# Kernel optimization log

Measured on AMD Instinct MI355X. Metric: run time of the kernel, lower is better.

The kernel has to match this reference:

```python
import jax, jax.numpy as jnp
import numpy as np

PI = 3.141592653589793
N, B, DIM, HEADS = 4, 8192, 1024, 4
HD = DIM // HEADS  # head_dim = 256


def setup_inputs() -> dict:
    key = jax.random.key(0)
    ks = jax.random.split(key, 10)
    glorot = jax.nn.initializers.glorot_uniform()
    return {
        "axis_embeddings": jax.random.normal(ks[0], (N, B, DIM), jnp.float32),
        "arg_embeddings": jax.random.uniform(ks[1], (N, B, DIM), jnp.float32),
        "W_axis1": glorot(ks[2], (HD, 2 * HD), jnp.float32),
        "b_axis1": jnp.zeros((HD,), jnp.float32),
        "W_arg1": glorot(ks[3], (HD, 2 * HD), jnp.float32),
        "b_arg1": jnp.zeros((HD,), jnp.float32),
        "W_axis2": glorot(ks[4], (HD, HD), jnp.float32),
        "b_axis2": jnp.zeros((HD,), jnp.float32),
        "W_arg2": glorot(ks[5], (HD, HD), jnp.float32),
        "b_arg2": jnp.zeros((HD,), jnp.float32),
    }


def _linear(x, W, b):
    return jnp.einsum('...i,oi->...o', x, W) + b


def reference(axis_embeddings, arg_embeddings, W_axis1, b_axis1, W_arg1, b_arg1,
              W_axis2, b_axis2, W_arg2, b_arg2):
    axis = axis_embeddings.reshape(N, B, HEADS, HD)
    arg = arg_embeddings.reshape(N, B, HEADS, HD)
    al = axis - arg / 2
    ah = axis + arg / 2
    logits = jnp.concatenate([al, ah], axis=-1)  # [N,B,H,2*HD]

    # axis branch: attention over N then circular mean via atan2-style correction
    axis_h1 = jax.nn.relu(_linear(logits, W_axis1, b_axis1))
    axis_attn = jax.nn.softmax(_linear(axis_h1, W_axis2, b_axis2), axis=0)
    x_emb = jnp.sum(axis_attn * jnp.cos(axis), axis=0)  # [B,H,HD]
    y_emb = jnp.sum(axis_attn * jnp.sin(axis), axis=0)
    x_emb = jnp.where(jnp.abs(x_emb) < 0.001, 0.001, x_emb)
    axis_out = jnp.arctan(y_emb / x_emb)
    ind_x = x_emb < 0
    ind_y = y_emb < 0
    ind_two = ind_x & jnp.logical_not(ind_y)
    ind_three = ind_x & ind_y
    axis_out = axis_out + PI * ind_two.astype(axis_out.dtype) - PI * ind_three.astype(axis_out.dtype)

    # arg branch: mean-pooled gate, min over N (dropout p=0 -> identity)
    arg_h1 = jax.nn.relu(_linear(logits, W_arg1, b_arg1))
    gate = jax.nn.sigmoid(_linear(jnp.mean(arg_h1, axis=0), W_arg2, b_arg2))
    arg_out = jnp.min(arg, axis=0) * gate

    return axis_out.reshape(B, DIM), arg_out.reshape(B, DIM)
```

## Files before the change

kernel.cpp:

```cpp
#include <hip/hip_runtime.h>


typedef __attribute__((ext_vector_type(8))) _Float16 f16x8;
typedef __attribute__((ext_vector_type(8))) float f32x8;
typedef __attribute__((ext_vector_type(4))) float f32x4;

#define BH 32768
#define OUT_ARG_OFF 8388608

#define O_WXA_H 0
#define O_WXA_L 65536
#define O_WXR_H 131072
#define O_WXR_L 196608
#define O_WRA_H 262144
#define O_WRR_H 327680
#define O_W2X_H 393216
#define O_W2X_L 458752
#define O_W2G_H 524288
#define WS_HALFS 589824

__device__ __forceinline__ void split16(float x, _Float16& hi, _Float16& lo) {
  float xs = x * 16.0f;
  _Float16 h = (_Float16)xs;
  hi = h;
  lo = (_Float16)(xs - (float)h);
}

__device__ __forceinline__ int fragidx(int o, int k) {
  int ct = o >> 4, kk = k >> 5, lg = (k >> 3) & 3, l15 = o & 15, j = k & 7;
  return (ct * 8 + kk) * 512 + (lg * 16 + l15) * 8 + j;
}

__global__ void combine_weights(const float* __restrict__ Wx1, const float* __restrict__ Wr1,
                                const float* __restrict__ W2x, const float* __restrict__ W2g,
                                _Float16* __restrict__ ws) {
  int i = blockIdx.x * 256 + threadIdx.x;
  int o = i >> 8, k = i & 255;
  int d = fragidx(o, k);
  float a = Wx1[o * 512 + k], b = Wx1[o * 512 + 256 + k];
  _Float16 h, l;
  split16(a + b, h, l);          ws[O_WXA_H + d] = h; ws[O_WXA_L + d] = l;
  split16(0.5f * (b - a), h, l); ws[O_WXR_H + d] = h; ws[O_WXR_L + d] = l;
  a = Wr1[o * 512 + k]; b = Wr1[o * 512 + 256 + k];
  ws[O_WRA_H + d] = (_Float16)((a + b) * 16.0f);
  ws[O_WRR_H + d] = (_Float16)((0.5f * (b - a)) * 16.0f);
  split16(W2x[o * 256 + k], h, l); ws[O_W2X_H + d] = h; ws[O_W2X_L + d] = l;
  ws[O_W2G_H + d] = (_Float16)(W2g[o * 256 + k] * 16.0f);
}

#define MFMA16 __builtin_amdgcn_mfma_f32_16x16x32_f16

__global__ __launch_bounds__(512, 2)
void cone_main(const float* __restrict__ axisF, const float* __restrict__ argF,
               const float* __restrict__ bx1, const float* __restrict__ br1,
               const float* __restrict__ bg2,
               const _Float16* __restrict__ ws, float* __restrict__ out)
{
  __shared__ __align__(16) _Float16 lds[32768];
  _Float16* bufAxH = lds;
  _Float16* bufAxL = lds + 8192;
  _Float16* bufArH = lds + 16384;
  _Float16* bufArL = lds + 24576;

  const int tid = threadIdx.x;
  const int w   = tid >> 6;
  const int l   = tid & 63;
  const int l15 = l & 15;
  const int lg  = l >> 4;
  int bid = blockIdx.x;
  bid = ((bid & 7) << 9) + (bid >> 3);
  const int g0 = bid << 3;
  const float s = 1.0f / 256.0f;

  {
    #pragma unroll
    for (int c = 0; c < 2; ++c) {
      const int i   = c * 512 + tid;
      const int row = i >> 5;
      const int col = (i & 31) * 8;
      const int gofs = ((row & 3) * BH + g0 + (row >> 2)) * 256 + col;
      f32x8 va = *(const f32x8*)(axisF + gofs);
      f32x8 vr = *(const f32x8*)(argF + gofs);
      f16x8 xh, xl, rh, rl;
      #pragma unroll
      for (int j = 0; j < 8; ++j) {
        _Float16 h, lo2;
        split16(va[j], h, lo2); xh[j] = h; xl[j] = lo2;
        split16(vr[j], h, lo2); rh[j] = h; rl[j] = lo2;
      }
      const int ad = row * 256 + (col ^ ((row & 7) << 3));
      *(f16x8*)(bufAxH + ad) = xh;
      *(f16x8*)(bufAxL + ad) = xl;
      *(f16x8*)(bufArH + ad) = rh;
      *(f16x8*)(bufArL + ad) = rl;
    }
  }
  __syncthreads();

  f32x4 acc1[2][2], accm[2][2];
  #pragma unroll
  for (int mt = 0; mt < 2; ++mt)
    #pragma unroll
    for (int nt = 0; nt < 2; ++nt) { acc1[mt][nt] = (f32x4){0,0,0,0}; accm[mt][nt] = (f32x4){0,0,0,0}; }

  const int ct0 = w << 1;

  #pragma unroll
  for (int kk = 0; kk < 8; ++kk) {
    f16x8 xh[2], xl[2], rh[2], rl[2];
    #pragma unroll
    for (int mt = 0; mt < 2; ++mt) {
      const int row = (mt << 4) + l15;
      const int ad  = row * 256 + ((((kk) << 5) + (lg << 3)) ^ ((row & 7) << 3));
      xh[mt] = *(const f16x8*)(bufAxH + ad);
      xl[mt] = *(const f16x8*)(bufAxL + ad);
      rh[mt] = *(const f16x8*)(bufArH + ad);
      rl[mt] = *(const f16x8*)(bufArL + ad);
    }
    #pragma unroll
    for (int nt = 0; nt < 2; ++nt) {
      const int fb = (((ct0 + nt) << 3) + kk) * 512 + l * 8;
      const f16x8 wxah = *(const f16x8*)(ws + O_WXA_H + fb);
      const f16x8 wxal = *(const f16x8*)(ws + O_WXA_L + fb);
      const f16x8 wraw = *(const f16x8*)(ws + O_WRA_H + fb);
      const f16x8 wxrh = *(const f16x8*)(ws + O_WXR_H + fb);
      const f16x8 wxrl = *(const f16x8*)(ws + O_WXR_L + fb);
      const f16x8 wrrw = *(const f16x8*)(ws + O_WRR_H + fb);
      __builtin_amdgcn_s_setprio(1);
      #pragma unroll
      for (int mt = 0; mt < 2; ++mt) {
        acc1[mt][nt] = MFMA16(xh[mt], wxah, acc1[mt][nt], 0, 0, 0);
        acc1[mt][nt] = MFMA16(xl[mt], wxah, acc1[mt][nt], 0, 0, 0);
        acc1[mt][nt] = MFMA16(xh[mt], wxal, acc1[mt][nt], 0, 0, 0);
        accm[mt][nt] = MFMA16(xh[mt], wraw, accm[mt][nt], 0, 0, 0);
        acc1[mt][nt] = MFMA16(rh[mt], wxrh, acc1[mt][nt], 0, 0, 0);
        acc1[mt][nt] = MFMA16(rl[mt], wxrh, acc1[mt][nt], 0, 0, 0);
        acc1[mt][nt] = MFMA16(rh[mt], wxrl, acc1[mt][nt], 0, 0, 0);
        accm[mt][nt] = MFMA16(rh[mt], wrrw, accm[mt][nt], 0, 0, 0);
      }
      __builtin_amdgcn_s_setprio(0);
    }
  }
  __syncthreads();

  _Float16* h1h = bufAxH;
  _Float16* h1l = bufAxL;
  _Float16* h1m = bufArH;
  if (tid < 256) *(f16x8*)(h1m + 2048 + tid * 8) = (f16x8){0,0,0,0,0,0,0,0};
  #pragma unroll
  for (int nt = 0; nt < 2; ++nt) {
    const int c  = (w << 5) + (nt << 4) + l15;
    const float bvx = bx1[c];
    const float bvr = br1[c];
    #pragma unroll
    for (int mt = 0; mt < 2; ++mt) {
      #pragma unroll
      for (int r = 0; r < 4; ++r) {
        const int row = (mt << 4) + (lg << 2) + r;
        const float v = fmaxf(acc1[mt][nt][r] * s + bvx, 0.f);
        _Float16 h, lo2; split16(v, h, lo2);
        const int ad = row * 256 + (c ^ ((row & 7) << 3));
        h1h[ad] = h; h1l[ad] = lo2;
      }
      const int p = (mt << 2) + lg;
      float sm = 0.f;
      #pragma unroll
      for (int r = 0; r < 4; ++r) sm += fmaxf(accm[mt][nt][r] * s + bvr, 0.f);
      h1m[p * 256 + (c ^ ((p & 7) << 3))] = (_Float16)(0.25f * sm * 16.0f);
    }
  }
  __syncthreads();

  f32x4 acc2[2][2];
  f32x4 acc3[2];
  #pragma unroll
  for (int mt = 0; mt < 2; ++mt) { acc2[mt][0] = (f32x4){0,0,0,0}; acc2[mt][1] = (f32x4){0,0,0,0}; }
  acc3[0] = (f32x4){0,0,0,0}; acc3[1] = (f32x4){0,0,0,0};
  {
    f16x8 wh[3][2], wl[3][2], wg[3][2];
    f16x8 a2h[2][2], a2l[2][2], am[2];
    #pragma unroll
    for (int p = 0; p < 2; ++p)
      #pragma unroll
      for (int nt = 0; nt < 2; ++nt) {
        const int fb = (((ct0 + nt) << 3) + p) * 512 + l * 8;
        wh[p][nt] = *(const f16x8*)(ws + O_W2X_H + fb);
        wl[p][nt] = *(const f16x8*)(ws + O_W2X_L + fb);
        wg[p][nt] = *(const f16x8*)(ws + O_W2G_H + fb);
      }
    #pragma unroll
    for (int mt = 0; mt < 2; ++mt) {
      const int row = (mt << 4) + l15;
      const int ad  = row * 256 + ((lg << 3) ^ ((row & 7) << 3));
      a2h[0][mt] = *(const f16x8*)(h1h + ad);
      a2l[0][mt] = *(const f16x8*)(h1l + ad);
    }
    am[0] = *(const f16x8*)(h1m + l15 * 256 + ((lg << 3) ^ ((l15 & 7) << 3)));
    #pragma unroll
    for (int kk = 0; kk < 8; ++kk) {
      const int cs = kk % 3, ns = (kk + 2) % 3, ab = kk & 1, an = ab ^ 1;
      if (kk < 6) {
        #pragma unroll
        for (int nt = 0; nt < 2; ++nt) {
          const int fb = (((ct0 + nt) << 3) + (kk + 2)) * 512 + l * 8;
          wh[ns][nt] = *(const f16x8*)(ws + O_W2X_H + fb);
          wl[ns][nt] = *(const f16x8*)(ws + O_W2X_L + fb);
          wg[ns][nt] = *(const f16x8*)(ws + O_W2G_H + fb);
        }
      }
      if (kk < 7) {
        #pragma unroll
        for (int mt = 0; mt < 2; ++mt) {
          const int row = (mt << 4) + l15;
          const int ad  = row * 256 + ((((kk + 1) << 5) + (lg << 3)) ^ ((row & 7) << 3));
          a2h[an][mt] = *(const f16x8*)(h1h + ad);
          a2l[an][mt] = *(const f16x8*)(h1l + ad);
        }
        am[an] = *(const f16x8*)(h1m + l15 * 256 + ((((kk + 1) << 5) + (lg << 3)) ^ ((l15 & 7) << 3)));
      }
      __builtin_amdgcn_s_setprio(1);
      #pragma unroll
      for (int nt = 0; nt < 2; ++nt) {
        #pragma unroll
        for (int mt = 0; mt < 2; ++mt) {
          acc2[mt][nt] = MFMA16(a2h[ab][mt], wh[cs][nt], acc2[mt][nt], 0, 0, 0);
          acc2[mt][nt] = MFMA16(a2l[ab][mt], wh[cs][nt], acc2[mt][nt], 0, 0, 0);
          acc2[mt][nt] = MFMA16(a2h[ab][mt], wl[cs][nt], acc2[mt][nt], 0, 0, 0);
        }
        acc3[nt] = MFMA16(am[ab], wg[cs][nt], acc3[nt], 0, 0, 0);
      }
      __builtin_amdgcn_s_setprio(0);
    }
  }

  #pragma unroll
  for (int nt = 0; nt < 2; ++nt) {
    const int c = (w << 5) + (nt << 4) + l15;
    #pragma unroll
    for (int mt = 0; mt < 2; ++mt) {
      float lv[4];
      #pragma unroll
      for (int r = 0; r < 4; ++r) lv[r] = acc2[mt][nt][r] * s;
      const float mx = fmaxf(fmaxf(lv[0], lv[1]), fmaxf(lv[2], lv[3]));
      float e[4]; float sum = 0.f;
      #pragma unroll
      for (int r = 0; r < 4; ++r) { e[r] = __expf(lv[r] - mx); sum += e[r]; }
      const float inv = 1.f / sum;
      const int g = g0 + (mt << 2) + lg;
      float x = 0.f, y = 0.f;
      #pragma unroll
      for (int r = 0; r < 4; ++r) {
        const float av = axisF[(r * BH + g) * 256 + c];
        float sn, cs2;
        __sincosf(av, &sn, &cs2);
        const float at = e[r] * inv;
        x += at * cs2;
        y += at * sn;
      }
      if (fabsf(x) < 0.001f) x = 0.001f;
      out[g * 256 + c] = atan2f(y, x);
    }
  }

  #pragma unroll
  for (int nt = 0; nt < 2; ++nt) {
    const int c = (w << 5) + (nt << 4) + l15;
    const float bgv = bg2[c];
    #pragma unroll
    for (int r = 0; r < 4; ++r) {
      const int p = (lg << 2) + r;
      if (p < 8) {
        const int g = g0 + p;
        const float gate = 1.f / (1.f + __expf(-(acc3[nt][r] * s + bgv)));
        float mn = argF[g * 256 + c];
        #pragma unroll
        for (int n = 1; n < 4; ++n)
          mn = fminf(mn, argF[(n * BH + g) * 256 + c]);
        out[OUT_ARG_OFF + g * 256 + c] = mn * gate;
      }
    }
  }
}

extern "C" void kernel_launch(void* const* d_in, const int* in_sizes, int n_in,
                              void* d_out, int out_size, void* d_ws, size_t ws_size,
                              hipStream_t stream) {
  const float* axisF = (const float*)d_in[0];
  const float* argF  = (const float*)d_in[1];
  const float* Wx1   = (const float*)d_in[2];
  const float* bx1   = (const float*)d_in[3];
  const float* Wr1   = (const float*)d_in[4];
  const float* br1   = (const float*)d_in[5];
  const float* W2x   = (const float*)d_in[6];
  const float* W2g   = (const float*)d_in[8];
  const float* bg2   = (const float*)d_in[9];
  float* out = (float*)d_out;
  _Float16* ws = (_Float16*)d_ws;

  combine_weights<<<256, 256, 0, stream>>>(Wx1, Wr1, W2x, W2g, ws);
  cone_main<<<4096, 512, 0, stream>>>(axisF, argF, bx1, br1, bg2, ws, out);
}
```

Before: 324.5 us.

## Switch main GEMMs to 32x32x16 MFMA tiles with new fragment layout

Reworks the first-layer and axis second-layer GEMMs to use 32x32x16 f16 MFMA instructions with a single 32x32 accumulator per wave, repacking weights into a 32-wide fragment layout and widening the LDS XOR swizzle to 32 rows. Weight fragments are double-buffered from global memory across the k loop, and epilogue global loads for axis and arg values are batched before use. The aim is fewer MFMA issues and fewer LDS fragment reads per unit of work, with better latency hiding. The bigger accumulators raise register pressure, and the new swizzle and layout must stay consistent between the staging writes and the fragment reads.

```diff
diff --git a/kernel.cpp b/kernel.cpp
--- a/kernel.cpp
+++ b/kernel.cpp
@@ -4,6 +4,7 @@
 typedef __attribute__((ext_vector_type(8))) _Float16 f16x8;
 typedef __attribute__((ext_vector_type(8))) float f32x8;
 typedef __attribute__((ext_vector_type(4))) float f32x4;
+typedef __attribute__((ext_vector_type(16))) float f32x16;
 
 #define BH 32768
 #define OUT_ARG_OFF 8388608
@@ -26,9 +27,11 @@
   lo = (_Float16)(xs - (float)h);
 }
 
-__device__ __forceinline__ int fragidx(int o, int k) {
-  int ct = o >> 4, kk = k >> 5, lg = (k >> 3) & 3, l15 = o & 15, j = k & 7;
-  return (ct * 8 + kk) * 512 + (lg * 16 + l15) * 8 + j;
+__device__ __forceinline__ int fragidx16(int o, int k) {
+  return ((o >> 4) * 8 + (k >> 5)) * 512 + ((((k >> 3) & 3) << 4) + (o & 15)) * 8 + (k & 7);
+}
+__device__ __forceinline__ int fragidx32(int o, int k) {
+  return ((o >> 5) * 16 + (k >> 4)) * 512 + ((((k >> 3) & 1) << 5) + (o & 31)) * 8 + (k & 7);
 }
 
 __global__ void combine_weights(const float* __restrict__ Wx1, const float* __restrict__ Wr1,
@@ -36,7 +39,7 @@
                                 _Float16* __restrict__ ws) {
   int i = blockIdx.x * 256 + threadIdx.x;
   int o = i >> 8, k = i & 255;
-  int d = fragidx(o, k);
+  int d = fragidx32(o, k);
   float a = Wx1[o * 512 + k], b = Wx1[o * 512 + 256 + k];
   _Float16 h, l;
   split16(a + b, h, l);          ws[O_WXA_H + d] = h; ws[O_WXA_L + d] = l;
@@ -45,10 +48,44 @@
   ws[O_WRA_H + d] = (_Float16)((a + b) * 16.0f);
   ws[O_WRR_H + d] = (_Float16)((0.5f * (b - a)) * 16.0f);
   split16(W2x[o * 256 + k], h, l); ws[O_W2X_H + d] = h; ws[O_W2X_L + d] = l;
-  ws[O_W2G_H + d] = (_Float16)(W2g[o * 256 + k] * 16.0f);
+  ws[O_W2G_H + fragidx16(o, k)] = (_Float16)(W2g[o * 256 + k] * 16.0f);
 }
 
 #define MFMA16 __builtin_amdgcn_mfma_f32_16x16x32_f16
+#define MFMA32 __builtin_amdgcn_mfma_f32_32x32x16_f16
+
+__device__ __forceinline__ void gemm1_pass32(const _Float16* __restrict__ ws,
+                                             int oBh, int oBl, int oBm,
+                                             const _Float16* bufH, const _Float16* bufL,
+                                             int w, int l,
+                                             f32x16& acc1, f32x16& accm) {
+  const int row = l & 31;
+  const int hi8 = (l >> 5) << 3;
+  f16x8 wh[2], wl[2], wm[2];
+  {
+    const int fb = (w * 16) * 512 + l * 8;
+    wh[0] = *(const f16x8*)(ws + oBh + fb);
+    wl[0] = *(const f16x8*)(ws + oBl + fb);
+    wm[0] = *(const f16x8*)(ws + oBm + fb);
+  }
+  #pragma unroll
+  for (int st = 0; st < 16; ++st) {
+    const int cur = st & 1, nx = cur ^ 1;
+    if (st < 15) {
+      const int fb = (w * 16 + st + 1) * 512 + l * 8;
+      wh[nx] = *(const f16x8*)(ws + oBh + fb);
+      wl[nx] = *(const f16x8*)(ws + oBl + fb);
+      wm[nx] = *(const f16x8*)(ws + oBm + fb);
+    }
+    const int ad = row * 256 + ((st * 16 + hi8) ^ ((row & 31) << 3));
+    const f16x8 ah = *(const f16x8*)(bufH + ad);
+    const f16x8 al = *(const f16x8*)(bufL + ad);
+    acc1 = MFMA32(ah, wh[cur], acc1, 0, 0, 0);
+    acc1 = MFMA32(al, wh[cur], acc1, 0, 0, 0);
+    acc1 = MFMA32(ah, wl[cur], acc1, 0, 0, 0);
+    accm = MFMA32(ah, wm[cur], accm, 0, 0, 0);
+  }
+}
 
 __global__ __launch_bounds__(512, 2)
 void cone_main(const float* __restrict__ axisF, const float* __restrict__ argF,
@@ -67,6 +104,8 @@
   const int l   = tid & 63;
   const int l15 = l & 15;
   const int lg  = l >> 4;
+  const int l31 = l & 31;
+  const int lh  = l >> 5;
   int bid = blockIdx.x;
   bid = ((bid & 7) << 9) + (bid >> 3);
   const int g0 = bid << 3;
@@ -88,7 +127,7 @@
         split16(va[j], h, lo2); xh[j] = h; xl[j] = lo2;
         split16(vr[j], h, lo2); rh[j] = h; rl[j] = lo2;
       }
-      const int ad = row * 256 + (col ^ ((row & 7) << 3));
+      const int ad = row * 256 + (col ^ ((row & 31) << 3));
       *(f16x8*)(bufAxH + ad) = xh;
       *(f16x8*)(bufAxL + ad) = xl;
       *(f16x8*)(bufArH + ad) = rh;
@@ -97,186 +136,150 @@
   }
   __syncthreads();
 
-  f32x4 acc1[2][2], accm[2][2];
+  f32x16 acc1, accm;
   #pragma unroll
-  for (int mt = 0; mt < 2; ++mt)
-    #pragma unroll
-    for (int nt = 0; nt < 2; ++nt) { acc1[mt][nt] = (f32x4){0,0,0,0}; accm[mt][nt] = (f32x4){0,0,0,0}; }
-
-  const int ct0 = w << 1;
-
-  #pragma unroll
-  for (int kk = 0; kk < 8; ++kk) {
-    f16x8 xh[2], xl[2], rh[2], rl[2];
-    #pragma unroll
-    for (int mt = 0; mt < 2; ++mt) {
-      const int row = (mt << 4) + l15;
-      const int ad  = row * 256 + ((((kk) << 5) + (lg << 3)) ^ ((row & 7) << 3));
-      xh[mt] = *(const f16x8*)(bufAxH + ad);
-      xl[mt] = *(const f16x8*)(bufAxL + ad);
-      rh[mt] = *(const f16x8*)(bufArH + ad);
-      rl[mt] = *(const f16x8*)(bufArL + ad);
-    }
-    #pragma unroll
-    for (int nt = 0; nt < 2; ++nt) {
-      const int fb = (((ct0 + nt) << 3) + kk) * 512 + l * 8;
-      const f16x8 wxah = *(const f16x8*)(ws + O_WXA_H + fb);
-      const f16x8 wxal = *(const f16x8*)(ws + O_WXA_L + fb);
-      const f16x8 wraw = *(const f16x8*)(ws + O_WRA_H + fb);
-      const f16x8 wxrh = *(const f16x8*)(ws + O_WXR_H + fb);
-      const f16x8 wxrl = *(const f16x8*)(ws + O_WXR_L + fb);
-      const f16x8 wrrw = *(const f16x8*)(ws + O_WRR_H + fb);
-      __builtin_amdgcn_s_setprio(1);
-      #pragma unroll
-      for (int mt = 0; mt < 2; ++mt) {
-        acc1[mt][nt] = MFMA16(xh[mt], wxah, acc1[mt][nt], 0, 0, 0);
-        acc1[mt][nt] = MFMA16(xl[mt], wxah, acc1[mt][nt], 0, 0, 0);
-        acc1[mt][nt] = MFMA16(xh[mt], wxal, acc1[mt][nt], 0, 0, 0);
-        accm[mt][nt] = MFMA16(xh[mt], wraw, accm[mt][nt], 0, 0, 0);
-        acc1[mt][nt] = MFMA16(rh[mt], wxrh, acc1[mt][nt], 0, 0, 0);
-        acc1[mt][nt] = MFMA16(rl[mt], wxrh, acc1[mt][nt], 0, 0, 0);
-        acc1[mt][nt] = MFMA16(rh[mt], wxrl, acc1[mt][nt], 0, 0, 0);
-        accm[mt][nt] = MFMA16(rh[mt], wrrw, accm[mt][nt], 0, 0, 0);
-      }
-      __builtin_amdgcn_s_setprio(0);
-    }
-  }
+  for (int i = 0; i < 16; ++i) { acc1[i] = 0.f; accm[i] = 0.f; }
+
+  gemm1_pass32(ws, O_WXA_H, O_WXA_L, O_WRA_H, bufAxH, bufAxL, w, l, acc1, accm);
+  gemm1_pass32(ws, O_WXR_H, O_WXR_L, O_WRR_H, bufArH, bufArL, w, l, acc1, accm);
   __syncthreads();
 
   _Float16* h1h = bufAxH;
   _Float16* h1l = bufAxL;
   _Float16* h1m = bufArH;
-  if (tid < 256) *(f16x8*)(h1m + 2048 + tid * 8) = (f16x8){0,0,0,0,0,0,0,0};
-  #pragma unroll
-  for (int nt = 0; nt < 2; ++nt) {
-    const int c  = (w << 5) + (nt << 4) + l15;
+  *(unsigned long long*)&h1m[2048 + tid * 4] = 0ull;
+  {
+    const int c = (w << 5) + l31;
     const float bvx = bx1[c];
     const float bvr = br1[c];
     #pragma unroll
-    for (int mt = 0; mt < 2; ++mt) {
-      #pragma unroll
-      for (int r = 0; r < 4; ++r) {
-        const int row = (mt << 4) + (lg << 2) + r;
-        const float v = fmaxf(acc1[mt][nt][r] * s + bvx, 0.f);
+    for (int g = 0; g < 4; ++g) {
+      float sm = 0.f;
+      #pragma unroll
+      for (int n = 0; n < 4; ++n) {
+        const int r = g * 4 + n;
+        const int row = (r & 3) + 8 * (r >> 2) + 4 * lh;
+        const float v = fmaxf(acc1[r] * s + bvx, 0.f);
         _Float16 h, lo2; split16(v, h, lo2);
-        const int ad = row * 256 + (c ^ ((row & 7) << 3));
+        const int ad = row * 256 + (c ^ ((row & 31) << 3));
         h1h[ad] = h; h1l[ad] = lo2;
-      }
-      const int p = (mt << 2) + lg;
-      float sm = 0.f;
-      #pragma unroll
-      for (int r = 0; r < 4; ++r) sm += fmaxf(accm[mt][nt][r] * s + bvr, 0.f);
+        sm += fmaxf(accm[r] * s + bvr, 0.f);
+      }
+      const int p = 2 * g + lh;
       h1m[p * 256 + (c ^ ((p & 7) << 3))] = (_Float16)(0.25f * sm * 16.0f);
     }
   }
   __syncthreads();
 
-  f32x4 acc2[2][2];
+  f32x16 acc2;
+  #pragma unroll
+  for (int i = 0; i < 16; ++i) acc2[i] = 0.f;
+  {
+    const int row = l31;
+    const int hi8 = lh << 3;
+    f16x8 w2h[2], w2l[2];
+    {
+      const int fb = (w * 16) * 512 + l * 8;
+      w2h[0] = *(const f16x8*)(ws + O_W2X_H + fb);
+      w2l[0] = *(const f16x8*)(ws + O_W2X_L + fb);
+    }
+    #pragma unroll
+    for (int st = 0; st < 16; ++st) {
+      const int cur = st & 1, nx = cur ^ 1;
+      if (st < 15) {
+        const int fb = (w * 16 + st + 1) * 512 + l * 8;
+        w2h[nx] = *(const f16x8*)(ws + O_W2X_H + fb);
+        w2l[nx] = *(const f16x8*)(ws + O_W2X_L + fb);
+      }
+      const int ad = row * 256 + ((st * 16 + hi8) ^ ((row & 31) << 3));
+      const f16x8 ah = *(const f16x8*)(h1h + ad);
+      const f16x8 al = *(const f16x8*)(h1l + ad);
+      acc2 = MFMA32(ah, w2h[cur], acc2, 0, 0, 0);
+      acc2 = MFMA32(al, w2h[cur], acc2, 0, 0, 0);
+      acc2 = MFMA32(ah, w2l[cur], acc2, 0, 0, 0);
+    }
+  }
+
   f32x4 acc3[2];
-  #pragma unroll
-  for (int mt = 0; mt < 2; ++mt) { acc2[mt][0] = (f32x4){0,0,0,0}; acc2[mt][1] = (f32x4){0,0,0,0}; }
-  acc3[0] = (f32x4){0,0,0,0}; acc3[1] = (f32x4){0,0,0,0};
-  {
-    f16x8 wh[3][2], wl[3][2], wg[3][2];
-    f16x8 a2h[2][2], a2l[2][2], am[2];
-    #pragma unroll
-    for (int p = 0; p < 2; ++p)
-      #pragma unroll
-      for (int nt = 0; nt < 2; ++nt) {
-        const int fb = (((ct0 + nt) << 3) + p) * 512 + l * 8;
-        wh[p][nt] = *(const f16x8*)(ws + O_W2X_H + fb);
-        wl[p][nt] = *(const f16x8*)(ws + O_W2X_L + fb);
-        wg[p][nt] = *(const f16x8*)(ws + O_W2G_H + fb);
-      }
-    #pragma unroll
-    for (int mt = 0; mt < 2; ++mt) {
-      const int row = (mt << 4) + l15;
-      const int ad  = row * 256 + ((lg << 3) ^ ((row & 7) << 3));
-      a2h[0][mt] = *(const f16x8*)(h1h + ad);
-      a2l[0][mt] = *(const f16x8*)(h1l + ad);
-    }
-    am[0] = *(const f16x8*)(h1m + l15 * 256 + ((lg << 3) ^ ((l15 & 7) << 3)));
+  acc3[0] = (f32x4){0, 0, 0, 0}; acc3[1] = (f32x4){0, 0, 0, 0};
+  {
+    f16x8 wg[2][2];
+    #pragma unroll
+    for (int nt = 0; nt < 2; ++nt)
+      wg[0][nt] = *(const f16x8*)(ws + O_W2G_H + (((w << 1) + nt) << 3) * 512 + l * 8);
     #pragma unroll
     for (int kk = 0; kk < 8; ++kk) {
-      const int cs = kk % 3, ns = (kk + 2) % 3, ab = kk & 1, an = ab ^ 1;
-      if (kk < 6) {
-        #pragma unroll
-        for (int nt = 0; nt < 2; ++nt) {
-          const int fb = (((ct0 + nt) << 3) + (kk + 2)) * 512 + l * 8;
-          wh[ns][nt] = *(const f16x8*)(ws + O_W2X_H + fb);
-          wl[ns][nt] = *(const f16x8*)(ws + O_W2X_L + fb);
-          wg[ns][nt] = *(const f16x8*)(ws + O_W2G_H + fb);
-        }
-      }
+      const int cur = kk & 1, nx = cur ^ 1;
       if (kk < 7) {
         #pragma unroll
-        for (int mt = 0; mt < 2; ++mt) {
-          const int row = (mt << 4) + l15;
-          const int ad  = row * 256 + ((((kk + 1) << 5) + (lg << 3)) ^ ((row & 7) << 3));
-          a2h[an][mt] = *(const f16x8*)(h1h + ad);
-          a2l[an][mt] = *(const f16x8*)(h1l + ad);
-        }
-        am[an] = *(const f16x8*)(h1m + l15 * 256 + ((((kk + 1) << 5) + (lg << 3)) ^ ((l15 & 7) << 3)));
-      }
-      __builtin_amdgcn_s_setprio(1);
-      #pragma unroll
-      for (int nt = 0; nt < 2; ++nt) {
-        #pragma unroll
-        for (int mt = 0; mt < 2; ++mt) {
-          acc2[mt][nt] = MFMA16(a2h[ab][mt], wh[cs][nt], acc2[mt][nt], 0, 0, 0);
-          acc2[mt][nt] = MFMA16(a2l[ab][mt], wh[cs][nt], acc2[mt][nt], 0, 0, 0);
-          acc2[mt][nt] = MFMA16(a2h[ab][mt], wl[cs][nt], acc2[mt][nt], 0, 0, 0);
-        }
-        acc3[nt] = MFMA16(am[ab], wg[cs][nt], acc3[nt], 0, 0, 0);
-      }
-      __builtin_amdgcn_s_setprio(0);
-    }
-  }
-
-  #pragma unroll
-  for (int nt = 0; nt < 2; ++nt) {
-    const int c = (w << 5) + (nt << 4) + l15;
-    #pragma unroll
-    for (int mt = 0; mt < 2; ++mt) {
+        for (int nt = 0; nt < 2; ++nt)
+          wg[nx][nt] = *(const f16x8*)(ws + O_W2G_H + ((((w << 1) + nt) << 3) + kk + 1) * 512 + l * 8);
+      }
+      const int k0 = (kk << 5) + (lg << 3);
+      const f16x8 am = *(const f16x8*)&h1m[l15 * 256 + (k0 ^ ((l15 & 7) << 3))];
+      acc3[0] = MFMA16(am, wg[cur][0], acc3[0], 0, 0, 0);
+      acc3[1] = MFMA16(am, wg[cur][1], acc3[1], 0, 0, 0);
+    }
+  }
+
+  {
+    const int c = (w << 5) + l31;
+    float av[4][4];
+    #pragma unroll
+    for (int g = 0; g < 4; ++g) {
+      const int gi = g0 + 2 * g + lh;
+      #pragma unroll
+      for (int n = 0; n < 4; ++n) av[g][n] = axisF[(n * BH + gi) * 256 + c];
+    }
+    #pragma unroll
+    for (int g = 0; g < 4; ++g) {
       float lv[4];
       #pragma unroll
-      for (int r = 0; r < 4; ++r) lv[r] = acc2[mt][nt][r] * s;
+      for (int n = 0; n < 4; ++n) lv[n] = acc2[g * 4 + n] * s;
       const float mx = fmaxf(fmaxf(lv[0], lv[1]), fmaxf(lv[2], lv[3]));
       float e[4]; float sum = 0.f;
       #pragma unroll
-      for (int r = 0; r < 4; ++r) { e[r] = __expf(lv[r] - mx); sum += e[r]; }
+      for (int n = 0; n < 4; ++n) { e[n] = __expf(lv[n] - mx); sum += e[n]; }
       const float inv = 1.f / sum;
-      const int g = g0 + (mt << 2) + lg;
       float x = 0.f, y = 0.f;
       #pragma unroll
-      for (int r = 0; r < 4; ++r) {
-        const float av = axisF[(r * BH + g) * 256 + c];
+      for (int n = 0; n < 4; ++n) {
         float sn, cs2;
-        __sincosf(av, &sn, &cs2);
-        const float at = e[r] * inv;
+        __sincosf(av[g][n], &sn, &cs2);
+        const float at = e[n] * inv;
         x += at * cs2;
         y += at * sn;
       }
       if (fabsf(x) < 0.001f) x = 0.001f;
-      out[g * 256 + c] = atan2f(y, x);
-    }
-  }
-
-  #pragma unroll
-  for (int nt = 0; nt < 2; ++nt) {
-    const int c = (w << 5) + (nt << 4) + l15;
-    const float bgv = bg2[c];
-    #pragma unroll
-    for (int r = 0; r < 4; ++r) {
-      const int p = (lg << 2) + r;
-      if (p < 8) {
-        const int g = g0 + p;
-        const float gate = 1.f / (1.f + __expf(-(acc3[nt][r] * s + bgv)));
-        float mn = argF[g * 256 + c];
-        #pragma unroll
-        for (int n = 1; n < 4; ++n)
-          mn = fminf(mn, argF[(n * BH + g) * 256 + c]);
-        out[OUT_ARG_OFF + g * 256 + c] = mn * gate;
+      const int gi = g0 + 2 * g + lh;
+      out[gi * 256 + c] = atan2f(y, x);
+    }
+  }
+
+  {
+    #pragma unroll
+    for (int nt = 0; nt < 2; ++nt) {
+      const int c = (w << 5) + (nt << 4) + l15;
+      const float bgv = bg2[c];
+      float ag[4][4];
+      #pragma unroll
+      for (int r = 0; r < 4; ++r) {
+        const int p = (lg << 2) + r;
+        if (p < 8) {
+          const int gi = g0 + p;
+          #pragma unroll
+          for (int n = 0; n < 4; ++n) ag[r][n] = argF[(n * BH + gi) * 256 + c];
+        }
+      }
+      #pragma unroll
+      for (int r = 0; r < 4; ++r) {
+        const int p = (lg << 2) + r;
+        if (p < 8) {
+          const int gi = g0 + p;
+          const float gate = 1.f / (1.f + __expf(-(acc3[nt][r] * s + bgv)));
+          const float mn = fminf(fminf(ag[r][0], ag[r][1]), fminf(ag[r][2], ag[r][3]));
+          out[OUT_ARG_OFF + gi * 256 + c] = mn * gate;
+        }
       }
     }
   }
```

After: 296.3 us. 1.1x faster.
